# Performance work log

Measured on AMD Instinct MI355X. Metric: run time of the kernel, lower is better.

## Reference

```python
import jax, jax.numpy as jnp
import numpy as np

B, S, D = 2, 2048, 1024
H, DH, DL, DR = 16, 64, 512, 64
DHID, N_SHARED, N_ROUTED, TOPK = 512, 2, 8, 2
EPS = 1e-6


def setup_inputs() -> dict:
    key = jax.random.key(0)
    ks = jax.random.split(key, 16)
    w = lambda k, shp: jax.random.normal(k, shp, dtype=jnp.float32) * 0.02
    return {
        "x": jax.random.normal(ks[0], (B, S, D), dtype=jnp.float32),
        "mask": jnp.tril(jnp.ones((S, S), dtype=bool)),  # causal
        "w_q": w(ks[1], (D, H * (DH + DR))),
        "w_dkv": w(ks[2], (D, DL)),
        "w_uk": w(ks[3], (DL, H * DH)),
        "w_uv": w(ks[4], (DL, H * DH)),
        "w_kr": w(ks[5], (D, DR)),
        "w_o": w(ks[6], (H * DH, D)),
        "attn_norm_w": jnp.ones((D,), jnp.float32),
        "mlp_norm_w": jnp.ones((D,), jnp.float32),
        "gate_w": w(ks[7], (D, N_ROUTED)),
        "wr_gate": w(ks[8], (N_ROUTED, D, DHID)),
        "wr_up": w(ks[9], (N_ROUTED, D, DHID)),
        "wr_down": w(ks[10], (N_ROUTED, DHID, D)),
        "ws_gate": w(ks[11], (N_SHARED, D, DHID)),
        "ws_up": w(ks[12], (N_SHARED, D, DHID)),
        "ws_down": w(ks[13], (N_SHARED, DHID, D)),
    }


def _rmsnorm(x, w):
    x32 = x.astype(jnp.float32)
    n = x32 * jax.lax.rsqrt(jnp.mean(x32 * x32, axis=-1, keepdims=True) + EPS)
    return n.astype(x.dtype) * w


def _rope_tables(seq_len, dim):
    half = dim // 2
    inv = 1.0 / (10000.0 ** (jnp.arange(half, dtype=jnp.float32) / half))
    ang = jnp.arange(seq_len, dtype=jnp.float32)[:, None] * inv[None, :]  # [S, dim/2]
    return jnp.cos(ang), jnp.sin(ang)


def _rope(t, cos, sin):
    # t: [..., S, dim]; rotate-half convention
    t1, t2 = jnp.split(t, 2, axis=-1)
    return jnp.concatenate([t1 * cos - t2 * sin, t2 * cos + t1 * sin], axis=-1)


def _layer(x, mask, w_q, w_dkv, w_uk, w_uv, w_kr, w_o, attn_norm_w, mlp_norm_w,
           gate_w, wr_gate, wr_up, wr_down, ws_gate, ws_up, ws_down):
    # ---- pre-norm MLA attention + residual ----
    h = _rmsnorm(x, attn_norm_w)
    cos, sin = _rope_tables(S, DR)

    q = (h @ w_q).reshape(B, S, H, DH + DR).transpose(0, 2, 1, 3)  # [B,H,S,DH+DR]
    q_c, q_r = q[..., :DH], _rope(q[..., DH:], cos, sin)

    latent = h @ w_dkv                                              # [B,S,DL]
    k_c = (latent @ w_uk).reshape(B, S, H, DH).transpose(0, 2, 1, 3)  # [B,H,S,DH]
    v = (latent @ w_uv).reshape(B, S, H, DH).transpose(0, 2, 1, 3)
    k_r = _rope(h @ w_kr, cos, sin)                                 # [B,S,DR] shared across heads

    scale = 1.0 / np.sqrt(DH + DR)
    scores = (jnp.einsum("bhqd,bhkd->bhqk", q_c, k_c)
              + jnp.einsum("bhqd,bkd->bhqk", q_r, k_r)) * scale
    scores = jnp.where(mask, scores, jnp.float32(-1e9))
    attn = jax.nn.softmax(scores, axis=-1)
    ctx = jnp.einsum("bhqk,bhkd->bhqd", attn, v)                    # [B,H,S,DH]
    attn_out = ctx.transpose(0, 2, 1, 3).reshape(B, S, H * DH) @ w_o
    x = x + attn_out

    # ---- pre-norm shared + routed MoE FFN + residual ----
    h = _rmsnorm(x, mlp_norm_w).reshape(-1, D)                      # [T,D]
    probs = jax.nn.softmax(h @ gate_w, axis=-1)                     # [T,NR]
    vals, idx = jax.lax.top_k(probs, TOPK)                          # [T,K]
    gw = vals / jnp.sum(vals, axis=-1, keepdims=True)
    dense_w = jnp.sum(jax.nn.one_hot(idx, N_ROUTED, dtype=h.dtype) * gw[..., None], axis=1)  # [T,NR]

    g = jax.nn.silu(jnp.einsum("td,edh->teh", h, wr_gate))
    u = jnp.einsum("td,edh->teh", h, wr_up)
    y = jnp.einsum("teh,ehd->ted", g * u, wr_down)                  # [T,NR,D]
    routed = jnp.einsum("ted,te->td", y, dense_w)

    gs = jax.nn.silu(jnp.einsum("td,sdh->tsh", h, ws_gate))
    us = jnp.einsum("td,sdh->tsh", h, ws_up)
    shared = jnp.einsum("tsh,shd->td", gs * us, ws_down)

    return x + (routed + shared).reshape(B, S, D)


def reference(x, mask, w_q, w_dkv, w_uk, w_uv, w_kr, w_o, attn_norm_w, mlp_norm_w,
              gate_w, wr_gate, wr_up, wr_down, ws_gate, ws_up, ws_down):
    return _layer(x, mask, w_q, w_dkv, w_uk, w_uv, w_kr, w_o, attn_norm_w, mlp_norm_w,
                  gate_w, wr_gate, wr_up, wr_down, ws_gate, ws_up, ws_down)
```

## Files before the change

kernel.cpp:

```cpp
#include <hip/hip_runtime.h>
#include <hip/hip_bf16.h>
#include <stdint.h>

typedef unsigned short u16;
typedef __attribute__((ext_vector_type(8))) short short8;
typedef __attribute__((ext_vector_type(4))) float f32x4;
typedef __attribute__((ext_vector_type(4))) int i32x4;
typedef __attribute__((ext_vector_type(2))) unsigned int u32x2;

#define B_    2
#define S_    2048
#define D_    1024
#define H_    16
#define T_    (B_*S_)

static __device__ __forceinline__ float b2f(u16 h) { return __uint_as_float(((uint32_t)h) << 16); }
static __device__ __forceinline__ u16 f2b(float f) {
    uint32_t u = __float_as_uint(f);
    u += 0x7fffu + ((u >> 16) & 1u);
    return (u16)(u >> 16);
}
static __device__ __forceinline__ uint32_t pack2(float a, float b) {
    return (uint32_t)f2b(a) | ((uint32_t)f2b(b) << 16);
}
#define MFMA(a,b,c) __builtin_amdgcn_mfma_f32_16x16x32_bf16(a,b,c,0,0,0)

static __device__ __forceinline__ void gl2lds16(const void* g, void* l) {
    __builtin_amdgcn_global_load_lds((const __attribute__((address_space(1))) void*)g,
                                     (__attribute__((address_space(3))) void*)l, 16, 0, 0);
}

__global__ __launch_bounds__(256) void transpose_cvt(const float* __restrict__ in,
    u16* __restrict__ out, int K, int N, long inEZ, long outEZ)
{
    __shared__ float tile[32][33];
    const int e = blockIdx.z;
    const float* ip = in + (long)e * inEZ;
    u16* op = out + (long)e * outEZ;
    int n0 = blockIdx.x * 32, k0 = blockIdx.y * 32;
    int tx = threadIdx.x, ty = threadIdx.y;
#pragma unroll
    for (int i = 0; i < 4; ++i) {
        int k = k0 + ty + 8 * i, n = n0 + tx;
        tile[ty + 8 * i][tx] = (k < K && n < N) ? ip[(long)k * N + n] : 0.f;
    }
    __syncthreads();
#pragma unroll
    for (int i = 0; i < 4; ++i) {
        int n = n0 + ty + 8 * i, k = k0 + tx;
        if (n < N && k < K) op[(long)n * K + k] = f2b(tile[tx][ty + 8 * i]);
    }
}

__global__ __launch_bounds__(256) void gemm_k(const u16* __restrict__ A, long lda,
    const u16* __restrict__ Bt, long ldb, void* __restrict__ Cv, long ldc, int K,
    int mode, const float* __restrict__ resid)
{
    __shared__ u16 As[128 * 32];
    __shared__ u16 Bs[128 * 32];
    const int tid = threadIdx.x, lane = tid & 63, wave = tid >> 6;
    const int wm = (wave & 1) * 64, wn = (wave >> 1) * 64;
    const int quad = lane >> 4, rr = lane & 15, q8 = quad * 8;
    const long row0 = (long)blockIdx.y * 128, col0 = (long)blockIdx.x * 128;
    f32x4 acc[4][4];
#pragma unroll
    for (int i = 0; i < 4; ++i)
#pragma unroll
        for (int j = 0; j < 4; ++j)
#pragma unroll
            for (int c = 0; c < 4; ++c) acc[i][j][c] = 0.f;
    const int band = wave * 32;
    const u16* ga = A + (row0 + band + (lane >> 2)) * lda + (lane & 3) * 8;
    const u16* gb = Bt + (col0 + band + (lane >> 2)) * ldb + (lane & 3) * 8;
    u16* la = &As[band * 32];
    u16* lb = &Bs[band * 32];
    for (int k0 = 0; k0 < K; k0 += 32) {
        gl2lds16(ga + k0, la);
        gl2lds16(ga + k0 + 16 * lda, la + 16 * 32);
        gl2lds16(gb + k0, lb);
        gl2lds16(gb + k0 + 16 * ldb, lb + 16 * 32);
        __syncthreads();
        short8 af[4], bf[4];
#pragma unroll
        for (int mi = 0; mi < 4; ++mi) af[mi] = *(const short8*)&As[(wm + mi * 16 + rr) * 32 + q8];
#pragma unroll
        for (int ni = 0; ni < 4; ++ni) bf[ni] = *(const short8*)&Bs[(wn + ni * 16 + rr) * 32 + q8];
#pragma unroll
        for (int mi = 0; mi < 4; ++mi)
#pragma unroll
            for (int ni = 0; ni < 4; ++ni)
                acc[mi][ni] = MFMA(af[mi], bf[ni], acc[mi][ni]);
        __syncthreads();
    }
#pragma unroll
    for (int mi = 0; mi < 4; ++mi)
#pragma unroll
        for (int ni = 0; ni < 4; ++ni)
#pragma unroll
            for (int rg = 0; rg < 4; ++rg) {
                long r = row0 + wm + mi * 16 + quad * 4 + rg;
                long c = col0 + wn + ni * 16 + rr;
                float v = acc[mi][ni][rg];
                if (mode == 1)      ((u16*)Cv)[r * ldc + c] = f2b(v);
                else if (mode == 2) ((float*)Cv)[r * ldc + c] += v;
                else                ((float*)Cv)[r * ldc + c] = v + resid[r * 1024 + c];
            }
}

__global__ __launch_bounds__(256) void gemm_gather(const u16* __restrict__ H2,
    const u16* __restrict__ BtAll, u16* __restrict__ C,
    const int* __restrict__ cnt, const int* __restrict__ off,
    const int* __restrict__ elist)
{
    const int e = blockIdx.z;
    const int cntE = cnt[e], offE = off[e];
    const int m0 = blockIdx.y * 128;
    if (m0 >= cntE) return;
    const u16* Bt = BtAll + (long)e * 1024 * 1024;
    __shared__ u16 As[128 * 32];
    __shared__ u16 Bs[128 * 32];
    const int tid = threadIdx.x, lane = tid & 63, wave = tid >> 6;
    const int wm = (wave & 1) * 64, wn = (wave >> 1) * 64;
    const int quad = lane >> 4, rr = lane & 15, q8 = quad * 8;
    const long col0 = (long)blockIdx.x * 128;
    f32x4 acc[4][4];
#pragma unroll
    for (int i = 0; i < 4; ++i)
#pragma unroll
        for (int j = 0; j < 4; ++j)
#pragma unroll
            for (int c = 0; c < 4; ++c) acc[i][j][c] = 0.f;
    const int band = wave * 32;
    int r0 = m0 + band + (lane >> 2);
    int r1 = r0 + 16;
    int tok0 = elist[offE + (r0 < cntE ? r0 : cntE - 1)];
    int tok1 = elist[offE + (r1 < cntE ? r1 : cntE - 1)];
    const u16* ga0 = H2 + (long)tok0 * 1024 + (lane & 3) * 8;
    const u16* ga1 = H2 + (long)tok1 * 1024 + (lane & 3) * 8;
    const u16* gb = Bt + (col0 + band + (lane >> 2)) * 1024L + (lane & 3) * 8;
    u16* la = &As[band * 32];
    u16* lb = &Bs[band * 32];
    for (int k0 = 0; k0 < 1024; k0 += 32) {
        gl2lds16(ga0 + k0, la);
        gl2lds16(ga1 + k0, la + 16 * 32);
        gl2lds16(gb + k0, lb);
        gl2lds16(gb + k0 + 16 * 1024, lb + 16 * 32);
        __syncthreads();
        short8 af[4], bf[4];
#pragma unroll
        for (int mi = 0; mi < 4; ++mi) af[mi] = *(const short8*)&As[(wm + mi * 16 + rr) * 32 + q8];
#pragma unroll
        for (int ni = 0; ni < 4; ++ni) bf[ni] = *(const short8*)&Bs[(wn + ni * 16 + rr) * 32 + q8];
#pragma unroll
        for (int mi = 0; mi < 4; ++mi)
#pragma unroll
            for (int ni = 0; ni < 4; ++ni)
                acc[mi][ni] = MFMA(af[mi], bf[ni], acc[mi][ni]);
        __syncthreads();
    }
#pragma unroll
    for (int mi = 0; mi < 4; ++mi)
#pragma unroll
        for (int ni = 0; ni < 4; ++ni)
#pragma unroll
            for (int rg = 0; rg < 4; ++rg) {
                int ml = wm + mi * 16 + quad * 4 + rg;
                long c = col0 + wn + ni * 16 + rr;
                if (m0 + ml < cntE)
                    C[(long)(offE + m0 + ml) * 1024 + c] = f2b(acc[mi][ni][rg]);
            }
}

__global__ __launch_bounds__(256) void gemm_slot(const u16* __restrict__ Act,
    const u16* __restrict__ BtAll, u16* __restrict__ rout,
    const int* __restrict__ cnt, const int* __restrict__ off)
{
    const int e = blockIdx.z;
    const int cntE = cnt[e], offE = off[e];
    const int m0 = blockIdx.y * 128;
    if (m0 >= cntE) return;
    const u16* Bt = BtAll + (long)e * 1024 * 512;
    __shared__ u16 As[128 * 32];
    __shared__ u16 Bs[128 * 32];
    const int tid = threadIdx.x, lane = tid & 63, wave = tid >> 6;
    const int wm = (wave & 1) * 64, wn = (wave >> 1) * 64;
    const int quad = lane >> 4, rr = lane & 15, q8 = quad * 8;
    const long col0 = (long)blockIdx.x * 128;
    f32x4 acc[4][4];
#pragma unroll
    for (int i = 0; i < 4; ++i)
#pragma unroll
        for (int j = 0; j < 4; ++j)
#pragma unroll
            for (int c = 0; c < 4; ++c) acc[i][j][c] = 0.f;
    const int band = wave * 32;
    int r0 = offE + m0 + band + (lane >> 2); if (r0 > 8191) r0 = 8191;
    int r1 = r0 + 16; if (r1 > 8191) r1 = 8191;
    const u16* ga0 = Act + (long)r0 * 1024 + (lane & 3) * 8;
    const u16* ga1 = Act + (long)r1 * 1024 + (lane & 3) * 8;
    const u16* gb = Bt + (col0 + band + (lane >> 2)) * 512L + (lane & 3) * 8;
    u16* la = &As[band * 32];
    u16* lb = &Bs[band * 32];
    for (int k0 = 0; k0 < 512; k0 += 32) {
        gl2lds16(ga0 + k0, la);
        gl2lds16(ga1 + k0, la + 16 * 32);
        gl2lds16(gb + k0, lb);
        gl2lds16(gb + k0 + 16 * 512, lb + 16 * 32);
        __syncthreads();
        short8 af[4], bf[4];
#pragma unroll
        for (int mi = 0; mi < 4; ++mi) af[mi] = *(const short8*)&As[(wm + mi * 16 + rr) * 32 + q8];
#pragma unroll
        for (int ni = 0; ni < 4; ++ni) bf[ni] = *(const short8*)&Bs[(wn + ni * 16 + rr) * 32 + q8];
#pragma unroll
        for (int mi = 0; mi < 4; ++mi)
#pragma unroll
            for (int ni = 0; ni < 4; ++ni)
                acc[mi][ni] = MFMA(af[mi], bf[ni], acc[mi][ni]);
        __syncthreads();
    }
#pragma unroll
    for (int mi = 0; mi < 4; ++mi)
#pragma unroll
        for (int ni = 0; ni < 4; ++ni)
#pragma unroll
            for (int rg = 0; rg < 4; ++rg) {
                int ml = wm + mi * 16 + quad * 4 + rg;
                long c = col0 + wn + ni * 16 + rr;
                if (m0 + ml < cntE)
                    rout[(long)(offE + m0 + ml) * 1024 + c] = f2b(acc[mi][ni][rg]);
            }
}

__global__ __launch_bounds__(256) void rmsnorm_wave(const float* __restrict__ x,
    const float* __restrict__ w, u16* __restrict__ out)
{
    const int t = blockIdx.x * 4 + (threadIdx.x >> 6);
    const int lane = threadIdx.x & 63;
    const float* xp = x + (size_t)t * D_;
    f32x4 v[4];
    float s = 0.f;
#pragma unroll
    for (int i = 0; i < 4; ++i) {
        v[i] = *(const f32x4*)&xp[lane * 4 + i * 256];
#pragma unroll
        for (int j = 0; j < 4; ++j) s += v[i][j] * v[i][j];
    }
#pragma unroll
    for (int o = 32; o > 0; o >>= 1) s += __shfl_xor(s, o);
    const float inv = rsqrtf(s * (1.f / D_) + 1e-6f);
    u16* op = out + (size_t)t * D_;
#pragma unroll
    for (int i = 0; i < 4; ++i) {
        const int d = lane * 4 + i * 256;
        f32x4 wv = *(const f32x4*)&w[d];
        u32x2 pk;
        pk[0] = pack2(v[i][0] * inv * wv[0], v[i][1] * inv * wv[1]);
        pk[1] = pack2(v[i][2] * inv * wv[2], v[i][3] * inv * wv[3]);
        *(u32x2*)&op[d] = pk;
    }
}

__global__ __launch_bounds__(256) void rmsnorm_gate_fused(const float* __restrict__ xm,
    const float* __restrict__ nw, const float* __restrict__ gw, u16* __restrict__ h2,
    int* __restrict__ tok_e, float* __restrict__ tok_w)
{
    const int t = blockIdx.x * 4 + (threadIdx.x >> 6);
    const int lane = threadIdx.x & 63;
    const float* xp = xm + (size_t)t * D_;
    f32x4 v[4];
    float s = 0.f;
#pragma unroll
    for (int i = 0; i < 4; ++i) {
        v[i] = *(const f32x4*)&xp[lane * 4 + i * 256];
#pragma unroll
        for (int j = 0; j < 4; ++j) s += v[i][j] * v[i][j];
    }
#pragma unroll
    for (int o = 32; o > 0; o >>= 1) s += __shfl_xor(s, o);
    const float inv = rsqrtf(s * (1.f / D_) + 1e-6f);
    u16* op = h2 + (size_t)t * D_;
    float part[8] = {0,0,0,0,0,0,0,0};
#pragma unroll
    for (int i = 0; i < 4; ++i) {
        const int d = lane * 4 + i * 256;
        f32x4 wv = *(const f32x4*)&nw[d];
        float hv[4];
#pragma unroll
        for (int j = 0; j < 4; ++j) hv[j] = v[i][j] * inv * wv[j];
        u32x2 pk;
        pk[0] = pack2(hv[0], hv[1]);
        pk[1] = pack2(hv[2], hv[3]);
        *(u32x2*)&op[d] = pk;
#pragma unroll
        for (int j = 0; j < 4; ++j) {
            const float* gp = gw + (size_t)(d + j) * 8;
#pragma unroll
            for (int e = 0; e < 8; ++e) part[e] += hv[j] * gp[e];
        }
    }
#pragma unroll
    for (int e = 0; e < 8; ++e)
#pragma unroll
        for (int o = 32; o > 0; o >>= 1) part[e] += __shfl_xor(part[e], o);
    if (lane == 0) {
        float mx = part[0];
#pragma unroll
        for (int e = 1; e < 8; ++e) mx = fmaxf(mx, part[e]);
        float p[8];
#pragma unroll
        for (int e = 0; e < 8; ++e) p[e] = __expf(part[e] - mx);
        int i0 = 0;
#pragma unroll
        for (int e = 1; e < 8; ++e) if (p[e] > p[i0]) i0 = e;
        int i1 = (i0 == 0) ? 1 : 0;
#pragma unroll
        for (int e = 0; e < 8; ++e) { if (e == i0) continue; if (p[e] > p[i1]) i1 = e; }
        float sw = p[i0] + p[i1];
        tok_e[2 * t] = i0;  tok_e[2 * t + 1] = i1;
        tok_w[2 * t] = p[i0] / sw;  tok_w[2 * t + 1] = p[i1] / sw;
    }
}

__global__ __launch_bounds__(256) void moe_route(const int* __restrict__ tok_e,
    int* __restrict__ cnt, int* __restrict__ off,
    int* __restrict__ elist, int* __restrict__ tslot)
{
    const int E = blockIdx.x;
    const int tid = threadIdx.x, lane = tid & 63, wave = tid >> 6;
    int ev[32];
#pragma unroll
    for (int i = 0; i < 8; ++i)
        *(i32x4*)&ev[i * 4] = *(const i32x4*)&tok_e[tid * 32 + i * 4];
    int c8[8] = {0,0,0,0,0,0,0,0};
#pragma unroll
    for (int k = 0; k < 32; ++k) ++c8[ev[k] & 7];
    int incl[8];
#pragma unroll
    for (int e = 0; e < 8; ++e) {
        int vv = c8[e];
#pragma unroll
        for (int d = 1; d < 64; d <<= 1) {
            int tmp = __shfl_up(vv, d);
            if (lane >= d) vv += tmp;
        }
        incl[e] = vv;
    }
    __shared__ int wtot[4][8];
    if (lane == 63)
#pragma unroll
        for (int e = 0; e < 8; ++e) wtot[wave][e] = incl[e];
    __syncthreads();
    int tot[8];
#pragma unroll
    for (int e = 0; e < 8; ++e) tot[e] = wtot[0][e] + wtot[1][e] + wtot[2][e] + wtot[3][e];
    int waveoff = 0;
    for (int w = 0; w < 4; ++w) if (w < wave) waveoff += wtot[w][E];
    int offE = 0;
#pragma unroll
    for (int e = 0; e < 8; ++e) if (e < E) offE += tot[e];
    int rank = offE + waveoff + (incl[E] - c8[E]);
#pragma unroll
    for (int k = 0; k < 32; ++k) {
        if ((ev[k] & 7) == E) {
            int p = tid * 32 + k;
            elist[rank] = p >> 1;
            tslot[p] = rank;
            ++rank;
        }
    }
    if (tid == 0) { cnt[E] = tot[E]; off[E] = offE; }
}

__global__ __launch_bounds__(256) void rope_q_kernel(u16* __restrict__ proj)
{
    int idx = blockIdx.x * 256 + threadIdx.x;
    int i  = idx & 31;
    int hh = (idx >> 5) & (H_ - 1);
    int t  = idx >> 9;
    int s  = t & (S_ - 1);
    float inv = __expf(-(float)i * 0.28782313662425575f);
    float ang = (float)s * inv;
    float c = cosf(ang), sn = sinf(ang);
    u16* base = proj + (size_t)t * 2688 + hh * 128 + 64;
    float t1 = b2f(base[i]), t2 = b2f(base[32 + i]);
    base[i]      = f2b(t1 * c - t2 * sn);
    base[32 + i] = f2b(t2 * c + t1 * sn);
}

__global__ __launch_bounds__(256) void rope_kr_kernel(u16* __restrict__ proj)
{
    int idx = blockIdx.x * 256 + threadIdx.x;
    int i = idx & 31;
    int t = idx >> 5;
    int s = t & (S_ - 1);
    float inv = __expf(-(float)i * 0.28782313662425575f);
    float ang = (float)s * inv;
    float c = cosf(ang), sn = sinf(ang);
    u16* base = proj + (size_t)t * 2688 + 2560;
    float t1 = b2f(base[i]), t2 = b2f(base[32 + i]);
    base[i]      = f2b(t1 * c - t2 * sn);
    base[32 + i] = f2b(t2 * c + t1 * sn);
}

#define KS  136
#define VS2 72
#define PS2 72
__global__ __launch_bounds__(256) void attn_flash(const u16* __restrict__ proj,
    const u16* __restrict__ kc, const u16* __restrict__ vt, u16* __restrict__ ctx)
{
    const int qidx = blockIdx.x >> 5;
    const int qt = (qidx < 8) ? (15 - qidx) : (qidx - 8);
    const int bh = blockIdx.x & 31;
    const int b = bh >> 4, h = bh & 15;
    const int q0 = qt * 128;
    const int tid = threadIdx.x, lane = tid & 63, wave = tid >> 6;
    const int quad = lane >> 4, rr = lane & 15, q8 = quad * 8;
    const int wm2 = wave * 32;

    __shared__ u16 Ks[64 * KS];
    __shared__ u16 Vs[64 * VS2];
    __shared__ u16 Ps[128 * PS2];

    const long tbase = (long)b * S_ + q0;
    short8 qf[2][4];
#pragma unroll
    for (int mi = 0; mi < 2; ++mi)
#pragma unroll
        for (int d0 = 0; d0 < 4; ++d0)
            qf[mi][d0] = *(const short8*)&proj[(tbase + wm2 + mi * 16 + rr) * 2688 + h * 128 + d0 * 32 + q8];

    f32x4 accO[2][4];
    float m_i[2], l_i[2];
#pragma unroll
    for (int mi = 0; mi < 2; ++mi) {
#pragma unroll
        for (int vi = 0; vi < 4; ++vi)
#pragma unroll
            for (int rg = 0; rg < 4; ++rg) accO[mi][vi][rg] = 0.f;
        m_i[mi] = -3e38f; l_i[mi] = 0.f;
    }
    const float sc = 0.08838834764831845f * 1.4426950408889634f;

    const int nkt = 2 * qt + 2;
    for (int kt = 0; kt < nkt; ++kt) {
        const int k0 = kt * 64;
        const long kb = (long)b * S_ + k0;
#pragma unroll
        for (int i = 0; i < 2; ++i) {
            int c = tid + i * 256, row = c >> 3, cc = (c & 7) * 8;
            *(short8*)&Ks[row * KS + cc] = *(const short8*)&kc[(kb + row) * 1024 + h * 64 + cc];
        }
#pragma unroll
        for (int i = 0; i < 2; ++i) {
            int c = tid + i * 256, row = c >> 3, cc = (c & 7) * 8;
            *(short8*)&Ks[row * KS + 64 + cc] = *(const short8*)&proj[(kb + row) * 2688 + 2560 + cc];
        }
#pragma unroll
        for (int i = 0; i < 2; ++i) {
            int c = tid + i * 256, row = c >> 3, cc = (c & 7) * 8;
            *(short8*)&Vs[row * VS2 + cc] =
                *(const short8*)&vt[(long)(h * 64 + row) * 4096 + b * 2048 + k0 + cc];
        }
        __syncthreads();

        const bool act0 = (k0 <= q0 + wm2 + 15);
        const bool act1 = (k0 <= q0 + wm2 + 31);
        f32x4 accS[2][4];
#pragma unroll
        for (int mi = 0; mi < 2; ++mi)
#pragma unroll
            for (int ki = 0; ki < 4; ++ki)
#pragma unroll
                for (int rg = 0; rg < 4; ++rg) accS[mi][ki][rg] = 0.f;
#pragma unroll
        for (int d0 = 0; d0 < 4; ++d0) {
            short8 kf[4];
#pragma unroll
            for (int ki = 0; ki < 4; ++ki) kf[ki] = *(const short8*)&Ks[(ki * 16 + rr) * KS + d0 * 32 + q8];
            if (act0) {
#pragma unroll
                for (int ki = 0; ki < 4; ++ki) accS[0][ki] = MFMA(kf[ki], qf[0][d0], accS[0][ki]);
            }
            if (act1) {
#pragma unroll
                for (int ki = 0; ki < 4; ++ki) accS[1][ki] = MFMA(kf[ki], qf[1][d0], accS[1][ki]);
            }
        }
#pragma unroll
        for (int mi = 0; mi < 2; ++mi) {
            if (!(mi ? act1 : act0)) continue;
            const int qg = q0 + wm2 + mi * 16 + rr;
            const bool maybe_mask = (k0 + 63 > q0 + wm2 + mi * 16);
            float mx = -3e38f;
#pragma unroll
            for (int ki = 0; ki < 4; ++ki)
#pragma unroll
                for (int rg = 0; rg < 4; ++rg) {
                    float w = accS[mi][ki][rg] * sc;
                    if (maybe_mask && (k0 + ki * 16 + quad * 4 + rg > qg)) w = -1e30f;
                    accS[mi][ki][rg] = w;
                    mx = fmaxf(mx, w);
                }
            mx = fmaxf(mx, __shfl_xor(mx, 16));
            mx = fmaxf(mx, __shfl_xor(mx, 32));
            float mnew = fmaxf(m_i[mi], mx);
            float alpha = exp2f(m_i[mi] - mnew);
            m_i[mi] = mnew;
            float ps = 0.f;
#pragma unroll
            for (int ki = 0; ki < 4; ++ki) {
                float p0 = exp2f(accS[mi][ki][0] - mnew);
                float p1 = exp2f(accS[mi][ki][1] - mnew);
                float p2 = exp2f(accS[mi][ki][2] - mnew);
                float p3 = exp2f(accS[mi][ki][3] - mnew);
                ps += (p0 + p1) + (p2 + p3);
                u32x2 pk; pk[0] = pack2(p0, p1); pk[1] = pack2(p2, p3);
                *(u32x2*)&Ps[(wm2 + mi * 16 + rr) * PS2 + ki * 16 + quad * 4] = pk;
            }
            ps += __shfl_xor(ps, 16);
            ps += __shfl_xor(ps, 32);
            l_i[mi] = l_i[mi] * alpha + ps;
#pragma unroll
            for (int vi = 0; vi < 4; ++vi)
#pragma unroll
                for (int rg = 0; rg < 4; ++rg) accO[mi][vi][rg] *= alpha;
        }
#pragma unroll
        for (int kc0 = 0; kc0 < 64; kc0 += 32) {
            short8 vf[4];
#pragma unroll
            for (int vi = 0; vi < 4; ++vi) vf[vi] = *(const short8*)&Vs[(vi * 16 + rr) * VS2 + kc0 + q8];
            if (act0) {
                short8 pf = *(const short8*)&Ps[(wm2 + rr) * PS2 + kc0 + q8];
#pragma unroll
                for (int vi = 0; vi < 4; ++vi) accO[0][vi] = MFMA(vf[vi], pf, accO[0][vi]);
            }
            if (act1) {
                short8 pf = *(const short8*)&Ps[(wm2 + 16 + rr) * PS2 + kc0 + q8];
#pragma unroll
                for (int vi = 0; vi < 4; ++vi) accO[1][vi] = MFMA(vf[vi], pf, accO[1][vi]);
            }
        }
        __syncthreads();
    }
#pragma unroll
    for (int mi = 0; mi < 2; ++mi) {
        float linv = 1.f / l_i[mi];
        long t = tbase + wm2 + mi * 16 + rr;
#pragma unroll
        for (int vi = 0; vi < 4; ++vi) {
            u32x2 pk;
            pk[0] = pack2(accO[mi][vi][0] * linv, accO[mi][vi][1] * linv);
            pk[1] = pack2(accO[mi][vi][2] * linv, accO[mi][vi][3] * linv);
            *(u32x2*)&ctx[t * 1024 + h * 64 + vi * 16 + quad * 4] = pk;
        }
    }
}

__global__ __launch_bounds__(256) void silu_mul(u16* __restrict__ gu, int nPairRows)
{
    int i = blockIdx.x * 256 + threadIdx.x;
    if (i >= nPairRows * 64) return;
    int row = i >> 6, j8 = (i & 63) * 8;
    long base = (long)row * 1024;
    short8 g8 = *(const short8*)&gu[base + j8];
    short8 u8 = *(const short8*)&gu[base + 512 + j8];
    short8 r;
#pragma unroll
    for (int j = 0; j < 8; ++j) {
        float g = b2f((u16)g8[j]), u = b2f((u16)u8[j]);
        r[j] = (short)f2b(g / (1.f + __expf(-g)) * u);
    }
    *(short8*)&gu[base + j8] = r;
}

__global__ __launch_bounds__(256) void final_kernel(const float* __restrict__ xm,
    const u16* __restrict__ rout, const int* __restrict__ tok_slot,
    const float* __restrict__ tok_w, float* __restrict__ out)
{
    long i = ((long)blockIdx.x * 256 + threadIdx.x) * 4;
    int t = (int)(i >> 10), d = (int)(i & 1023);
    int s0 = tok_slot[2 * t], s1 = tok_slot[2 * t + 1];
    float w0 = tok_w[2 * t], w1 = tok_w[2 * t + 1];
    f32x4 xv = *(const f32x4*)&xm[i];
    u32x2 r0 = *(const u32x2*)&rout[(long)s0 * 1024 + d];
    u32x2 r1 = *(const u32x2*)&rout[(long)s1 * 1024 + d];
    f32x4 o;
    o[0] = xv[0] + w0 * b2f((u16)(r0[0] & 0xffffu)) + w1 * b2f((u16)(r1[0] & 0xffffu));
    o[1] = xv[1] + w0 * b2f((u16)(r0[0] >> 16))     + w1 * b2f((u16)(r1[0] >> 16));
    o[2] = xv[2] + w0 * b2f((u16)(r0[1] & 0xffffu)) + w1 * b2f((u16)(r1[1] & 0xffffu));
    o[3] = xv[3] + w0 * b2f((u16)(r0[1] >> 16))     + w1 * b2f((u16)(r1[1] >> 16));
    *(f32x4*)&out[i] = o;
}

#define OFF_XMID   0UL
#define OFF_H      16777216UL
#define OFF_PROJ   25165824UL
#define OFF_WGU    25165824UL
#define OFF_KC     47185920UL
#define OFF_WD     47185920UL
#define OFF_VT     55574528UL
#define OFF_GUR    57671680UL
#define OFF_CTX    63963136UL
#define OFF_WATT   72351744UL
#define OFF_ROUT   74448896UL
#define OFF_GUS    91226112UL
#define OFF_TOKE   108003328UL
#define OFF_TOKW   108036096UL
#define OFF_TSLOT  108068864UL
#define OFF_ELIST  108101632UL
#define OFF_META   108134400UL

extern "C" void kernel_launch(void* const* d_in, const int* in_sizes, int n_in,
                              void* d_out, int out_size, void* d_ws, size_t ws_size,
                              hipStream_t stream)
{
    const float* x       = (const float*)d_in[0];
    const float* w_q     = (const float*)d_in[2];
    const float* w_dkv   = (const float*)d_in[3];
    const float* w_uk    = (const float*)d_in[4];
    const float* w_uv    = (const float*)d_in[5];
    const float* w_kr    = (const float*)d_in[6];
    const float* w_o     = (const float*)d_in[7];
    const float* attn_nw = (const float*)d_in[8];
    const float* mlp_nw  = (const float*)d_in[9];
    const float* gate_w  = (const float*)d_in[10];
    const float* wr_gate = (const float*)d_in[11];
    const float* wr_up   = (const float*)d_in[12];
    const float* wr_down = (const float*)d_in[13];
    const float* ws_gate = (const float*)d_in[14];
    const float* ws_up   = (const float*)d_in[15];
    const float* ws_down = (const float*)d_in[16];
    float* out = (float*)d_out;

    char* W = (char*)d_ws;
    float* x_mid = (float*)(W + OFF_XMID);
    u16* h      = (u16*)(W + OFF_H);
    u16* h2     = (u16*)(W + OFF_H);
    u16* proj   = (u16*)(W + OFF_PROJ);
    u16* wgu_t  = (u16*)(W + OFF_WGU);
    u16* kc     = (u16*)(W + OFF_KC);
    u16* wd_t   = (u16*)(W + OFF_WD);
    u16* vt     = (u16*)(W + OFF_VT);
    u16* gu_r   = (u16*)(W + OFF_GUR);
    u16* ctx    = (u16*)(W + OFF_CTX);
    u16* wqkv_t = (u16*)(W + OFF_WATT);
    u16* wuk_t  = wqkv_t + 2688 * 1024;
    u16* wuv_t  = wuk_t + 1024 * 512;
    u16* wo_t   = wuv_t + 1024 * 512;
    u16* rout   = (u16*)(W + OFF_ROUT);
    u16* gu_s   = (u16*)(W + OFF_GUS);
    int*   tok_e = (int*)(W + OFF_TOKE);
    float* tok_w = (float*)(W + OFF_TOKW);
    int*   tslot = (int*)(W + OFF_TSLOT);
    int*   elist = (int*)(W + OFF_ELIST);
    int*   meta  = (int*)(W + OFF_META);
    int* cnt = meta, * off = meta + 8;

    dim3 tb(32, 8);
    transpose_cvt<<<dim3(64, 32, 1), tb, 0, stream>>>(w_q,   wqkv_t,               1024, 2048, 0, 0);
    transpose_cvt<<<dim3(16, 32, 1), tb, 0, stream>>>(w_dkv, wqkv_t + 2048 * 1024, 1024, 512,  0, 0);
    transpose_cvt<<<dim3(2,  32, 1), tb, 0, stream>>>(w_kr,  wqkv_t + 2560 * 1024, 1024, 64,   0, 0);
    transpose_cvt<<<dim3(32, 16, 1), tb, 0, stream>>>(w_uk,  wuk_t,                512,  1024, 0, 0);
    transpose_cvt<<<dim3(32, 16, 1), tb, 0, stream>>>(w_uv,  wuv_t,                512,  1024, 0, 0);
    transpose_cvt<<<dim3(32, 32, 1), tb, 0, stream>>>(w_o,   wo_t,                 1024, 1024, 0, 0);

    rmsnorm_wave<<<T_ / 4, 256, 0, stream>>>(x, attn_nw, h);
    gemm_k<<<dim3(21, 32), 256, 0, stream>>>(h, 1024, wqkv_t, 1024, proj, 2688, 1024, 1, nullptr);
    rope_q_kernel<<<(T_ * H_ * 32) / 256, 256, 0, stream>>>(proj);
    rope_kr_kernel<<<(T_ * 32) / 256, 256, 0, stream>>>(proj);
    gemm_k<<<dim3(8, 32), 256, 0, stream>>>(proj + 2048, 2688, wuk_t, 512, kc, 1024, 512, 1, nullptr);
    gemm_k<<<dim3(32, 8), 256, 0, stream>>>(wuv_t, 512, proj + 2048, 2688, vt, 4096, 512, 1, nullptr);
    attn_flash<<<512, 256, 0, stream>>>(proj, kc, vt, ctx);
    gemm_k<<<dim3(8, 32), 256, 0, stream>>>(ctx, 1024, wo_t, 1024, x_mid, 1024, 1024, 3, x);

    transpose_cvt<<<dim3(16, 32, 8), tb, 0, stream>>>(wr_gate, wgu_t,              1024, 512, 524288, 1048576);
    transpose_cvt<<<dim3(16, 32, 8), tb, 0, stream>>>(wr_up,   wgu_t + 512 * 1024, 1024, 512, 524288, 1048576);
    transpose_cvt<<<dim3(16, 32, 2), tb, 0, stream>>>(ws_gate, wgu_t + 8 * 1048576,              1024, 512, 524288, 1048576);
    transpose_cvt<<<dim3(16, 32, 2), tb, 0, stream>>>(ws_up,   wgu_t + 8 * 1048576 + 512 * 1024, 1024, 512, 524288, 1048576);
    transpose_cvt<<<dim3(32, 16, 8), tb, 0, stream>>>(wr_down, wd_t,               512, 1024, 524288, 524288);
    transpose_cvt<<<dim3(32, 16, 2), tb, 0, stream>>>(ws_down, wd_t + 8 * 524288,  512, 1024, 524288, 524288);

    rmsnorm_gate_fused<<<T_ / 4, 256, 0, stream>>>(x_mid, mlp_nw, gate_w, h2, tok_e, tok_w);
    moe_route<<<8, 256, 0, stream>>>(tok_e, cnt, off, elist, tslot);
    gemm_gather<<<dim3(8, 64, 8), 256, 0, stream>>>(h2, wgu_t, gu_r, cnt, off, elist);
    silu_mul<<<(8192 * 64) / 256, 256, 0, stream>>>(gu_r, 8192);
    gemm_slot<<<dim3(8, 64, 8), 256, 0, stream>>>(gu_r, wd_t, rout, cnt, off);
    gemm_k<<<dim3(16, 32), 256, 0, stream>>>(h2, 1024, wgu_t + 8 * 1048576, 1024, gu_s, 2048, 1024, 1, nullptr);
    silu_mul<<<(8192 * 64) / 256, 256, 0, stream>>>(gu_s, 8192);
    gemm_k<<<dim3(8, 32), 256, 0, stream>>>(gu_s, 2048, wd_t + 8 * 524288, 512, x_mid, 1024, 512, 2, nullptr);
    gemm_k<<<dim3(8, 32), 256, 0, stream>>>(gu_s + 1024, 2048, wd_t + 9 * 524288, 512, x_mid, 1024, 512, 2, nullptr);
    final_kernel<<<(T_ * D_) / 1024, 256, 0, stream>>>(x_mid, rout, tslot, tok_w, out);
}
```

Measured before the change: 631.9 us.

## Shrink attention query tile to 64 rows and load V directly into registers

The flash attention kernel now uses 64-query tiles with one 16-row slice per wave instead of 128-query tiles, launching twice as many blocks. V fragments are read straight from global memory into registers instead of being staged through LDS. The causal mask runs only on the diagonal tile, rescaling is skipped when no row max changes, and the P conversion uses a packed hardware bf16 convert. This aims to improve load balance and occupancy and to cut LDS traffic, at the cost of re-reading K per smaller tile and uncoalesced global V loads.

```diff
diff --git a/kernel.cpp b/kernel.cpp
--- a/kernel.cpp
+++ b/kernel.cpp
@@ -22,6 +22,11 @@
 }
 static __device__ __forceinline__ uint32_t pack2(float a, float b) {
     return (uint32_t)f2b(a) | ((uint32_t)f2b(b) << 16);
+}
+static __device__ __forceinline__ uint32_t cvtpk(float a, float b) {
+    uint32_t r;
+    asm("v_cvt_pk_bf16_f32 %0, %1, %2" : "=v"(r) : "v"(a), "v"(b));
+    return r;
 }
 #define MFMA(a,b,c) __builtin_amdgcn_mfma_f32_16x16x32_bf16(a,b,c,0,0,0)
 
@@ -404,45 +409,39 @@
 }
 
 #define KS  136
-#define VS2 72
 #define PS2 72
 __global__ __launch_bounds__(256) void attn_flash(const u16* __restrict__ proj,
     const u16* __restrict__ kc, const u16* __restrict__ vt, u16* __restrict__ ctx)
 {
     const int qidx = blockIdx.x >> 5;
-    const int qt = (qidx < 8) ? (15 - qidx) : (qidx - 8);
+    const int qt = (qidx < 16) ? (31 - qidx) : (qidx - 16);
     const int bh = blockIdx.x & 31;
     const int b = bh >> 4, h = bh & 15;
-    const int q0 = qt * 128;
+    const int q0 = qt * 64;
     const int tid = threadIdx.x, lane = tid & 63, wave = tid >> 6;
     const int quad = lane >> 4, rr = lane & 15, q8 = quad * 8;
-    const int wm2 = wave * 32;
+    const int wm2 = wave * 16;
 
     __shared__ u16 Ks[64 * KS];
-    __shared__ u16 Vs[64 * VS2];
-    __shared__ u16 Ps[128 * PS2];
+    __shared__ u16 Ps[64 * PS2];
 
     const long tbase = (long)b * S_ + q0;
-    short8 qf[2][4];
-#pragma unroll
-    for (int mi = 0; mi < 2; ++mi)
-#pragma unroll
-        for (int d0 = 0; d0 < 4; ++d0)
-            qf[mi][d0] = *(const short8*)&proj[(tbase + wm2 + mi * 16 + rr) * 2688 + h * 128 + d0 * 32 + q8];
-
-    f32x4 accO[2][4];
-    float m_i[2], l_i[2];
-#pragma unroll
-    for (int mi = 0; mi < 2; ++mi) {
-#pragma unroll
-        for (int vi = 0; vi < 4; ++vi)
-#pragma unroll
-            for (int rg = 0; rg < 4; ++rg) accO[mi][vi][rg] = 0.f;
-        m_i[mi] = -3e38f; l_i[mi] = 0.f;
-    }
+    short8 qf[4];
+#pragma unroll
+    for (int d0 = 0; d0 < 4; ++d0)
+        qf[d0] = *(const short8*)&proj[(tbase + wm2 + rr) * 2688 + h * 128 + d0 * 32 + q8];
+
+    f32x4 accO[4];
+    float m_i = -3e38f, l_i = 0.f;
+#pragma unroll
+    for (int vi = 0; vi < 4; ++vi)
+#pragma unroll
+        for (int rg = 0; rg < 4; ++rg) accO[vi][rg] = 0.f;
     const float sc = 0.08838834764831845f * 1.4426950408889634f;
 
-    const int nkt = 2 * qt + 2;
+    const u16* vbase = vt + (size_t)(h * 64 + rr) * 4096 + b * 2048 + q8;
+
+    const int nkt = qt + 1;
     for (int kt = 0; kt < nkt; ++kt) {
         const int k0 = kt * 64;
         const long kb = (long)b * S_ + k0;
@@ -456,103 +455,94 @@
             int c = tid + i * 256, row = c >> 3, cc = (c & 7) * 8;
             *(short8*)&Ks[row * KS + 64 + cc] = *(const short8*)&proj[(kb + row) * 2688 + 2560 + cc];
         }
-#pragma unroll
-        for (int i = 0; i < 2; ++i) {
-            int c = tid + i * 256, row = c >> 3, cc = (c & 7) * 8;
-            *(short8*)&Vs[row * VS2 + cc] =
-                *(const short8*)&vt[(long)(h * 64 + row) * 4096 + b * 2048 + k0 + cc];
-        }
-        __syncthreads();
-
-        const bool act0 = (k0 <= q0 + wm2 + 15);
-        const bool act1 = (k0 <= q0 + wm2 + 31);
-        f32x4 accS[2][4];
-#pragma unroll
-        for (int mi = 0; mi < 2; ++mi)
-#pragma unroll
-            for (int ki = 0; ki < 4; ++ki)
-#pragma unroll
-                for (int rg = 0; rg < 4; ++rg) accS[mi][ki][rg] = 0.f;
+        __syncthreads();
+
+        f32x4 accS[4];
+#pragma unroll
+        for (int ki = 0; ki < 4; ++ki)
+#pragma unroll
+            for (int rg = 0; rg < 4; ++rg) accS[ki][rg] = 0.f;
 #pragma unroll
         for (int d0 = 0; d0 < 4; ++d0) {
             short8 kf[4];
 #pragma unroll
             for (int ki = 0; ki < 4; ++ki) kf[ki] = *(const short8*)&Ks[(ki * 16 + rr) * KS + d0 * 32 + q8];
-            if (act0) {
-#pragma unroll
-                for (int ki = 0; ki < 4; ++ki) accS[0][ki] = MFMA(kf[ki], qf[0][d0], accS[0][ki]);
-            }
-            if (act1) {
-#pragma unroll
-                for (int ki = 0; ki < 4; ++ki) accS[1][ki] = MFMA(kf[ki], qf[1][d0], accS[1][ki]);
-            }
-        }
-#pragma unroll
-        for (int mi = 0; mi < 2; ++mi) {
-            if (!(mi ? act1 : act0)) continue;
-            const int qg = q0 + wm2 + mi * 16 + rr;
-            const bool maybe_mask = (k0 + 63 > q0 + wm2 + mi * 16);
-            float mx = -3e38f;
+#pragma unroll
+            for (int ki = 0; ki < 4; ++ki) accS[ki] = MFMA(kf[ki], qf[d0], accS[ki]);
+        }
+        __syncthreads();
+
+        short8 vf0[4], vf1[4];
+#pragma unroll
+        for (int vi = 0; vi < 4; ++vi) {
+            vf0[vi] = *(const short8*)(vbase + (size_t)vi * 16 * 4096 + k0);
+            vf1[vi] = *(const short8*)(vbase + (size_t)vi * 16 * 4096 + k0 + 32);
+        }
+
+        float mx = -3e38f;
+        if (kt == qt) {
+            const int qg = q0 + wm2 + rr;
 #pragma unroll
             for (int ki = 0; ki < 4; ++ki)
 #pragma unroll
                 for (int rg = 0; rg < 4; ++rg) {
-                    float w = accS[mi][ki][rg] * sc;
-                    if (maybe_mask && (k0 + ki * 16 + quad * 4 + rg > qg)) w = -1e30f;
-                    accS[mi][ki][rg] = w;
+                    float w = accS[ki][rg] * sc;
+                    if (k0 + ki * 16 + quad * 4 + rg > qg) w = -1e30f;
+                    accS[ki][rg] = w;
                     mx = fmaxf(mx, w);
                 }
-            mx = fmaxf(mx, __shfl_xor(mx, 16));
-            mx = fmaxf(mx, __shfl_xor(mx, 32));
-            float mnew = fmaxf(m_i[mi], mx);
-            float alpha = exp2f(m_i[mi] - mnew);
-            m_i[mi] = mnew;
-            float ps = 0.f;
-#pragma unroll
-            for (int ki = 0; ki < 4; ++ki) {
-                float p0 = exp2f(accS[mi][ki][0] - mnew);
-                float p1 = exp2f(accS[mi][ki][1] - mnew);
-                float p2 = exp2f(accS[mi][ki][2] - mnew);
-                float p3 = exp2f(accS[mi][ki][3] - mnew);
-                ps += (p0 + p1) + (p2 + p3);
-                u32x2 pk; pk[0] = pack2(p0, p1); pk[1] = pack2(p2, p3);
-                *(u32x2*)&Ps[(wm2 + mi * 16 + rr) * PS2 + ki * 16 + quad * 4] = pk;
-            }
-            ps += __shfl_xor(ps, 16);
-            ps += __shfl_xor(ps, 32);
-            l_i[mi] = l_i[mi] * alpha + ps;
+        } else {
+#pragma unroll
+            for (int ki = 0; ki < 4; ++ki)
+#pragma unroll
+                for (int rg = 0; rg < 4; ++rg) {
+                    float w = accS[ki][rg] * sc;
+                    accS[ki][rg] = w;
+                    mx = fmaxf(mx, w);
+                }
+        }
+        mx = fmaxf(mx, __shfl_xor(mx, 16));
+        mx = fmaxf(mx, __shfl_xor(mx, 32));
+        if (__any(mx > m_i)) {
+            float mnew = fmaxf(m_i, mx);
+            float alpha = exp2f(m_i - mnew);
+            m_i = mnew;
+            l_i *= alpha;
 #pragma unroll
             for (int vi = 0; vi < 4; ++vi)
 #pragma unroll
-                for (int rg = 0; rg < 4; ++rg) accO[mi][vi][rg] *= alpha;
-        }
-#pragma unroll
-        for (int kc0 = 0; kc0 < 64; kc0 += 32) {
-            short8 vf[4];
-#pragma unroll
-            for (int vi = 0; vi < 4; ++vi) vf[vi] = *(const short8*)&Vs[(vi * 16 + rr) * VS2 + kc0 + q8];
-            if (act0) {
-                short8 pf = *(const short8*)&Ps[(wm2 + rr) * PS2 + kc0 + q8];
-#pragma unroll
-                for (int vi = 0; vi < 4; ++vi) accO[0][vi] = MFMA(vf[vi], pf, accO[0][vi]);
-            }
-            if (act1) {
-                short8 pf = *(const short8*)&Ps[(wm2 + 16 + rr) * PS2 + kc0 + q8];
-#pragma unroll
-                for (int vi = 0; vi < 4; ++vi) accO[1][vi] = MFMA(vf[vi], pf, accO[1][vi]);
-            }
-        }
-        __syncthreads();
-    }
-#pragma unroll
-    for (int mi = 0; mi < 2; ++mi) {
-        float linv = 1.f / l_i[mi];
-        long t = tbase + wm2 + mi * 16 + rr;
+                for (int rg = 0; rg < 4; ++rg) accO[vi][rg] *= alpha;
+        }
+        float ps = 0.f;
+#pragma unroll
+        for (int ki = 0; ki < 4; ++ki) {
+            float p0 = exp2f(accS[ki][0] - m_i);
+            float p1 = exp2f(accS[ki][1] - m_i);
+            float p2 = exp2f(accS[ki][2] - m_i);
+            float p3 = exp2f(accS[ki][3] - m_i);
+            ps += (p0 + p1) + (p2 + p3);
+            u32x2 pk; pk[0] = cvtpk(p0, p1); pk[1] = cvtpk(p2, p3);
+            *(u32x2*)&Ps[(wm2 + rr) * PS2 + ki * 16 + quad * 4] = pk;
+        }
+        ps += __shfl_xor(ps, 16);
+        ps += __shfl_xor(ps, 32);
+        l_i += ps;
+
+        short8 pf0 = *(const short8*)&Ps[(wm2 + rr) * PS2 + q8];
+        short8 pf1 = *(const short8*)&Ps[(wm2 + rr) * PS2 + 32 + q8];
+#pragma unroll
+        for (int vi = 0; vi < 4; ++vi) accO[vi] = MFMA(vf0[vi], pf0, accO[vi]);
+#pragma unroll
+        for (int vi = 0; vi < 4; ++vi) accO[vi] = MFMA(vf1[vi], pf1, accO[vi]);
+    }
+    {
+        float linv = 1.f / l_i;
+        long t = tbase + wm2 + rr;
 #pragma unroll
         for (int vi = 0; vi < 4; ++vi) {
             u32x2 pk;
-            pk[0] = pack2(accO[mi][vi][0] * linv, accO[mi][vi][1] * linv);
-            pk[1] = pack2(accO[mi][vi][2] * linv, accO[mi][vi][3] * linv);
+            pk[0] = pack2(accO[vi][0] * linv, accO[vi][1] * linv);
+            pk[1] = pack2(accO[vi][2] * linv, accO[vi][3] * linv);
             *(u32x2*)&ctx[t * 1024 + h * 64 + vi * 16 + quad * 4] = pk;
         }
     }
@@ -672,7 +662,7 @@
     rope_kr_kernel<<<(T_ * 32) / 256, 256, 0, stream>>>(proj);
     gemm_k<<<dim3(8, 32), 256, 0, stream>>>(proj + 2048, 2688, wuk_t, 512, kc, 1024, 512, 1, nullptr);
     gemm_k<<<dim3(32, 8), 256, 0, stream>>>(wuv_t, 512, proj + 2048, 2688, vt, 4096, 512, 1, nullptr);
-    attn_flash<<<512, 256, 0, stream>>>(proj, kc, vt, ctx);
+    attn_flash<<<1024, 256, 0, stream>>>(proj, kc, vt, ctx);
     gemm_k<<<dim3(8, 32), 256, 0, stream>>>(ctx, 1024, wo_t, 1024, x_mid, 1024, 1024, 3, x);
 
     transpose_cvt<<<dim3(16, 32, 8), tb, 0, stream>>>(wr_gate, wgu_t,              1024, 512, 524288, 1048576);
```

After: 622.5 us. About the same (-1.5%).
